# Kernel tuning notes

Measured on AMD Instinct MI355X. Metric: run time of the kernel, lower is better.

Reference implementation:

```python
import jax, jax.numpy as jnp
import numpy as np

NS, NW, E, DIN, OUT, H = 100_000, 400_000, 500_000, 64, 64, 4


def setup_inputs() -> dict:
    key = jax.random.key(0)
    ks = jax.random.split(key, 26)
    s = 1.0 / np.sqrt(DIN)
    sg = 1.0 / np.sqrt(OUT)
    inp = {
        "x_sites": jax.random.normal(ks[0], (NS, DIN), jnp.float32),
        "x_wells": jax.random.normal(ks[1], (NW, DIN), jnp.float32),
        "edge_sw_src": jax.random.randint(ks[2], (E,), 0, NS, jnp.int32),
        "edge_sw_dst": jax.random.randint(ks[3], (E,), 0, NW, jnp.int32),
        "edge_ws_src": jax.random.randint(ks[4], (E,), 0, NW, jnp.int32),
        "edge_ws_dst": jax.random.randint(ks[5], (E,), 0, NS, jnp.int32),
        # GAT ('pfas_sites','distance','gw_wells'), heads=4, concat=False
        "W_sw": jax.random.normal(ks[6], (DIN, H * OUT), jnp.float32) * s,
        "att_src_sw": jax.random.normal(ks[7], (H, OUT), jnp.float32) * sg,
        "att_dst_sw": jax.random.normal(ks[8], (H, OUT), jnp.float32) * sg,
        "b_sw": jnp.zeros((OUT,), jnp.float32),
        # SAGE ('gw_wells','distance','pfas_sites')
        "Wl_ws": jax.random.normal(ks[9], (DIN, OUT), jnp.float32) * s,
        "bl_ws": jnp.zeros((OUT,), jnp.float32),
        "Wr_ws": jax.random.normal(ks[10], (DIN, OUT), jnp.float32) * s,
        # GAT ('pfas_sites','self_loop','pfas_sites'), add_self_loops=True -> identity edges
        "W_ss": jax.random.normal(ks[11], (DIN, H * OUT), jnp.float32) * s,
        "att_src_ss": jax.random.normal(ks[12], (H, OUT), jnp.float32) * sg,
        "att_dst_ss": jax.random.normal(ks[13], (H, OUT), jnp.float32) * sg,
        "b_ss": jnp.zeros((OUT,), jnp.float32),
        # SAGE ('gw_wells','self_loop','gw_wells') with identity edges
        "Wl_ww": jax.random.normal(ks[14], (DIN, OUT), jnp.float32) * s,
        "bl_ww": jnp.zeros((OUT,), jnp.float32),
        "Wr_ww": jax.random.normal(ks[15], (DIN, OUT), jnp.float32) * s,
        # output heads
        "Wg": jax.random.normal(ks[16], (OUT, 1), jnp.float32) * sg,
        "bg": jnp.zeros((1,), jnp.float32),
        "Wsit": jax.random.normal(ks[17], (OUT, 1), jnp.float32) * sg,
        "bsit": jnp.zeros((1,), jnp.float32),
    }
    return inp


def _gat(x_src, x_dst, src, dst, W, a_src, a_dst, b, n_dst):
    """PyG GATConv, concat=False (mean over heads), negative_slope=0.2."""
    h, c = a_src.shape
    xs = (x_src @ W).reshape(-1, h, c)  # [Ns,H,C]
    xd = (x_dst @ W).reshape(-1, h, c)  # [Nd,H,C]
    al_s = jnp.einsum("nhc,hc->nh", xs, a_src)
    al_d = jnp.einsum("nhc,hc->nh", xd, a_dst)
    e = jax.nn.leaky_relu(al_s[src] + al_d[dst], 0.2)  # [E,H]
    m = jax.ops.segment_max(e, dst, num_segments=n_dst)
    ex = jnp.exp(e - m[dst])
    denom = jax.ops.segment_sum(ex, dst, num_segments=n_dst)
    alpha = ex / denom[dst]  # edge-softmax per dst node
    msg = xs[src] * alpha[:, :, None]  # [E,H,C] dominant intermediate
    out = jax.ops.segment_sum(msg, dst, num_segments=n_dst)
    return out.mean(axis=1) + b


def _sage(x_src, x_dst, src, dst, Wl, bl, Wr, n_dst):
    """PyG SAGEConv, mean aggregation, root_weight=True."""
    ssum = jax.ops.segment_sum(x_src[src], dst, num_segments=n_dst)
    cnt = jax.ops.segment_sum(jnp.ones((src.shape[0],), x_src.dtype), dst, num_segments=n_dst)
    mean = ssum / jnp.maximum(cnt, 1.0)[:, None]  # empty neighborhood -> 0 (PyG mean scatter)
    return mean @ Wl + bl + x_dst @ Wr


def reference(x_sites, x_wells, edge_sw_src, edge_sw_dst, edge_ws_src, edge_ws_dst,
              W_sw, att_src_sw, att_dst_sw, b_sw, Wl_ws, bl_ws, Wr_ws,
              W_ss, att_src_ss, att_dst_ss, b_ss, Wl_ww, bl_ww, Wr_ww,
              Wg, bg, Wsit, bsit):
    # relation 1: GAT sites -> wells
    gw = _gat(x_sites, x_wells, edge_sw_src, edge_sw_dst, W_sw, att_src_sw, att_dst_sw, b_sw, NW)
    # relation 4: SAGE self-loop on wells; identity edges -> mean == x itself
    gw = gw + (x_wells @ Wl_ww + bl_ww + x_wells @ Wr_ww)  # HeteroConv aggr='sum'
    # relation 2: SAGE wells -> sites
    si = _sage(x_wells, x_sites, edge_ws_src, edge_ws_dst, Wl_ws, bl_ws, Wr_ws, NS)
    # relation 3: GAT self-loop on sites (add_self_loops=True -> identity edge set);
    # softmax over a single self edge is 1, so output = mean over heads of lin(x) + bias
    si = si + (x_sites @ W_ss).reshape(NS, H, OUT).mean(axis=1) + b_ss
    # post: relu -> dropout (eval mode: identity) -> linear -> leaky_relu(0.01)
    gw = jax.nn.relu(gw)
    si = jax.nn.relu(si)
    o_gw = jax.nn.leaky_relu(gw @ Wg + bg, 0.01)   # [NW, 1]
    o_si = jax.nn.leaky_relu(si @ Wsit + bsit, 0.01)  # [NS, 1]
    return o_gw, o_si
```

## Files before the change

kernel.cpp:

```cpp
#include <hip/hip_runtime.h>

#define NS_ 100000
#define NW_ 400000
#define NE_ 500000
#define EPB 2048

typedef float f32x4_t __attribute__((ext_vector_type(4)));
typedef unsigned u32x4_t __attribute__((ext_vector_type(4)));

__device__ __forceinline__ float lrelu02(float x) { return x > 0.f ? x : 0.2f * x; }
__device__ __forceinline__ float bf2f(unsigned short u) {
    return __uint_as_float(((unsigned)u) << 16);
}
__device__ __forceinline__ unsigned short f2bf(float f) {
    unsigned u = __float_as_uint(f);
    u += 0x7FFFu + ((u >> 16) & 1u);
    return (unsigned short)(u >> 16);
}
__device__ __forceinline__ unsigned pk(float lo, float hi) {
    return (unsigned)f2bf(lo) | ((unsigned)f2bf(hi) << 16);
}
__device__ __forceinline__ void mfma_bf16(f32x4_t& acc, u32x4_t a, u32x4_t b) {
    asm volatile("v_mfma_f32_16x16x32_bf16 %0, %1, %2, %0" : "+v"(acc) : "v"(a), "v"(b));
}

__global__ void __launch_bounds__(256)
k_prep(const float* __restrict__ W_sw, const float* __restrict__ att_src,
       const float* __restrict__ att_dst,
       const float* __restrict__ Wl_ww, const float* __restrict__ Wr_ww,
       const float* __restrict__ Wl_ws, const float* __restrict__ Wr_ws,
       const float* __restrict__ W_ss,
       float* __restrict__ vd, float* __restrict__ vs,
       u32x4_t* __restrict__ fw, u32x4_t* __restrict__ fs,
       u32x4_t* __restrict__ fsp)
{
    const int tid = threadIdx.x;
    {
        int d = tid >> 2, h = tid & 3;
        const float4* wp = (const float4*)(W_sw + d * 256 + h * 64);
        const float4* ad = (const float4*)(att_dst + h * 64);
        const float4* as = (const float4*)(att_src + h * 64);
        float accd = 0.f, accs = 0.f;
#pragma unroll
        for (int c = 0; c < 16; ++c) {
            float4 wv = wp[c]; float4 dv = ad[c]; float4 sv = as[c];
            accd += wv.x * dv.x + wv.y * dv.y + wv.z * dv.z + wv.w * dv.w;
            accs += wv.x * sv.x + wv.y * sv.y + wv.z * sv.z + wv.w * sv.w;
        }
        vd[d * 4 + h] = accd;
        vs[d * 4 + h] = accs;
    }
    for (int idx = tid; idx < 512; idx += 256) {
        int f = idx >> 6, lane = idx & 63;
        int kc = f >> 2, ct = f & 3, q = lane >> 4, n = lane & 15;
        int c = ct * 16 + n;
        u32x4_t d;
#pragma unroll
        for (int i = 0; i < 4; ++i) {
            int k = kc * 32 + q * 8 + 2 * i;
            d[i] = pk(Wl_ww[k * 64 + c] + Wr_ww[k * 64 + c],
                      Wl_ww[(k + 1) * 64 + c] + Wr_ww[(k + 1) * 64 + c]);
        }
        fw[idx] = d;
    }
    for (int idx = tid; idx < 1024; idx += 256) {
        int f = idx >> 6, lane = idx & 63;
        int kc = f >> 2, ct = f & 3, q = lane >> 4, n = lane & 15;
        int c = ct * 16 + n;
        u32x4_t d;
#pragma unroll
        for (int i = 0; i < 4; ++i) {
            int k = kc * 32 + q * 8 + 2 * i;
            float lo, hi;
            if (k < 64) {
                lo = Wl_ws[k * 64 + c];
                hi = Wl_ws[(k + 1) * 64 + c];
            } else {
                int kk = k - 64;
                lo = Wr_ws[kk * 64 + c] + 0.25f * (W_ss[kk * 256 + c] + W_ss[kk * 256 + 64 + c] +
                                                   W_ss[kk * 256 + 128 + c] + W_ss[kk * 256 + 192 + c]);
                hi = Wr_ws[(kk + 1) * 64 + c] + 0.25f * (W_ss[(kk + 1) * 256 + c] + W_ss[(kk + 1) * 256 + 64 + c] +
                                                         W_ss[(kk + 1) * 256 + 128 + c] + W_ss[(kk + 1) * 256 + 192 + c]);
            }
            d[i] = pk(lo, hi);
        }
        fs[idx] = d;
    }
    for (int idx = tid; idx < 2048; idx += 256) {
        int f = idx >> 6, lane = idx & 63;
        int kc = f >> 4, ct = f & 15, q = lane >> 4, n = lane & 15;
        int c = ct * 16 + n;
        u32x4_t d;
#pragma unroll
        for (int i = 0; i < 4; ++i) {
            int k = kc * 32 + q * 8 + 2 * i;
            d[i] = pk(W_sw[k * 256 + c], W_sw[(k + 1) * 256 + c]);
        }
        fsp[idx] = d;
    }
}

#define SP_PAD 264
__global__ void __launch_bounds__(256)
k_sites_pre(const float* __restrict__ x_sites, const u32x4_t* __restrict__ fsp,
            const float* __restrict__ vs, unsigned short* __restrict__ xs,
            float* __restrict__ al_s)
{
    __shared__ unsigned short stg[4][16 * SP_PAD];
    __shared__ float vsl[256];
    const int tid = threadIdx.x;
    vsl[tid] = vs[tid];
    __syncthreads();
    const int wave = __builtin_amdgcn_readfirstlane(tid >> 6);
    const int lane = tid & 63, q = lane >> 4, n = lane & 15;
    const int sbase = blockIdx.x * 64 + wave * 16;
    const int srow = min(sbase + n, NS_ - 1);
    const float* xr = x_sites + (size_t)srow * 64 + q * 8;
    float4 x0 = *(const float4*)(xr);
    float4 x1 = *(const float4*)(xr + 4);
    float4 x2 = *(const float4*)(xr + 32);
    float4 x3 = *(const float4*)(xr + 36);
    u32x4_t am0 = { pk(x0.x, x0.y), pk(x0.z, x0.w), pk(x1.x, x1.y), pk(x1.z, x1.w) };
    u32x4_t am1 = { pk(x2.x, x2.y), pk(x2.z, x2.w), pk(x3.x, x3.y), pk(x3.z, x3.w) };
    float pa[4];
#pragma unroll
    for (int h = 0; h < 4; ++h) {
        const float* v0 = &vsl[(q * 8) * 4 + h];
        const float* v1 = &vsl[(32 + q * 8) * 4 + h];
        pa[h] = x0.x * v0[0]  + x0.y * v0[4]  + x0.z * v0[8]  + x0.w * v0[12]
              + x1.x * v0[16] + x1.y * v0[20] + x1.z * v0[24] + x1.w * v0[28]
              + x2.x * v1[0]  + x2.y * v1[4]  + x2.z * v1[8]  + x2.w * v1[12]
              + x3.x * v1[16] + x3.y * v1[20] + x3.z * v1[24] + x3.w * v1[28];
    }
#pragma unroll
    for (int h = 0; h < 4; ++h) {
        pa[h] += __shfl_xor(pa[h], 16, 64);
        pa[h] += __shfl_xor(pa[h], 32, 64);
    }
    if (q == 0 && sbase + n < NS_)
        *(float4*)(al_s + (size_t)(sbase + n) * 4) = make_float4(pa[0], pa[1], pa[2], pa[3]);

    f32x4_t acc[16];
#pragma unroll
    for (int ct = 0; ct < 16; ++ct) acc[ct] = (f32x4_t){0, 0, 0, 0};
    asm volatile("s_nop 3" : "+v"(am0), "+v"(am1));
#pragma unroll
    for (int ct = 0; ct < 16; ++ct) mfma_bf16(acc[ct], am0, fsp[ct * 64 + lane]);
#pragma unroll
    for (int ct = 0; ct < 16; ++ct) mfma_bf16(acc[ct], am1, fsp[(16 + ct) * 64 + lane]);
    asm volatile("s_nop 7\n\ts_nop 7" ::: "memory");
    unsigned short* ss = &stg[wave][0];
#pragma unroll
    for (int ct = 0; ct < 16; ++ct)
#pragma unroll
        for (int reg = 0; reg < 4; ++reg)
            ss[(q * 4 + reg) * SP_PAD + ct * 16 + n] = f2bf(acc[ct][reg]);
    __builtin_amdgcn_s_waitcnt(0);
#pragma unroll
    for (int i = 0; i < 8; ++i) {
        int g = i * 64 + lane;
        int r = g >> 5, c = g & 31;
        if (sbase + r < NS_) {
            u32x4_t v = *(const u32x4_t*)(ss + r * SP_PAD + c * 8);
            *(u32x4_t*)(xs + (size_t)(sbase + r) * 256 + c * 8) = v;
        }
    }
}

__global__ void __launch_bounds__(256)
k_hist2(const int* __restrict__ d1, int* __restrict__ h1,
        const int* __restrict__ d2, int* __restrict__ h2)
{
    int e = blockIdx.x * 256 + threadIdx.x;
    if (e >= NE_) return;
    if (blockIdx.y == 0) atomicAdd(&h1[d1[e]], 1);
    else                 atomicAdd(&h2[d2[e]], 1);
}

__global__ void __launch_bounds__(256)
k_scan1_2(const int* __restrict__ h1, int n1, int* __restrict__ b1, int nb1,
          const int* __restrict__ h2, int n2, int* __restrict__ b2)
{
    __shared__ int red[256];
    const int tid = threadIdx.x;
    const int bx = blockIdx.x;
    const int* hist; int n; int* bsum; int blk;
    if (bx < nb1) { hist = h1; n = n1; bsum = b1; blk = bx; }
    else          { hist = h2; n = n2; bsum = b2; blk = bx - nb1; }
    int base = blk * EPB + tid * 8;
    int s = 0;
#pragma unroll
    for (int i = 0; i < 8; ++i) { int idx = base + i; if (idx < n) s += hist[idx]; }
    red[tid] = s;
    __syncthreads();
    for (int off = 128; off > 0; off >>= 1) {
        if (tid < off) red[tid] += red[tid + off];
        __syncthreads();
    }
    if (tid == 0) bsum[blk] = red[0];
}

__global__ void __launch_bounds__(256)
k_scan2_2(int* __restrict__ b1, int nb1, int* __restrict__ b2, int nb2)
{
    __shared__ int sh[256];
    const int tid = threadIdx.x;
    int* bsum = blockIdx.x == 0 ? b1 : b2;
    int nb = blockIdx.x == 0 ? nb1 : nb2;
    sh[tid] = (tid < nb) ? bsum[tid] : 0;
    __syncthreads();
    for (int off = 1; off < 256; off <<= 1) {
        int u = (tid >= off) ? sh[tid - off] : 0;
        __syncthreads();
        sh[tid] += u;
        __syncthreads();
    }
    if (tid < nb) bsum[tid] = (tid == 0) ? 0 : sh[tid - 1];
}

__global__ void __launch_bounds__(256)
k_scan3_2(const int* __restrict__ h1, int n1, const int* __restrict__ b1,
          int* __restrict__ rp1, int* __restrict__ cu1, int nb1,
          const int* __restrict__ h2, int n2, const int* __restrict__ b2,
          int* __restrict__ rp2, int* __restrict__ cu2)
{
    __shared__ int tsum[256];
    const int tid = threadIdx.x;
    const int bx = blockIdx.x;
    const int* hist; int n; const int* bsum; int* rowptr; int* cursor; int blk;
    if (bx < nb1) { hist = h1; n = n1; bsum = b1; rowptr = rp1; cursor = cu1; blk = bx; }
    else          { hist = h2; n = n2; bsum = b2; rowptr = rp2; cursor = cu2; blk = bx - nb1; }
    int base = blk * EPB + tid * 8;
    int v[8]; int s = 0;
#pragma unroll
    for (int i = 0; i < 8; ++i) {
        int idx = base + i;
        v[i] = (idx < n) ? hist[idx] : 0;
        s += v[i];
    }
    tsum[tid] = s;
    __syncthreads();
    for (int off = 1; off < 256; off <<= 1) {
        int u = (tid >= off) ? tsum[tid - off] : 0;
        __syncthreads();
        tsum[tid] += u;
        __syncthreads();
    }
    int texcl = tsum[tid] - s;
    int run = bsum[blk] + texcl;
#pragma unroll
    for (int i = 0; i < 8; ++i) {
        int idx = base + i;
        if (idx < n) { rowptr[idx] = run; cursor[idx] = run; run += v[i]; }
    }
    if (blk == 0 && tid == 0) rowptr[n] = NE_;
}

__global__ void __launch_bounds__(256)
k_scatter2(const int* __restrict__ s1, const int* __restrict__ d1,
           int* __restrict__ c1, int* __restrict__ o1,
           const int* __restrict__ s2, const int* __restrict__ d2,
           int* __restrict__ c2, int* __restrict__ o2)
{
    int e = blockIdx.x * 256 + threadIdx.x;
    if (e >= NE_) return;
    if (blockIdx.y == 0) { int p = atomicAdd(&c1[d1[e]], 1); o1[p] = s1[e]; }
    else                 { int p = atomicAdd(&c2[d2[e]], 1); o2[p] = s2[e]; }
}

__global__ void __launch_bounds__(256)
k_gat_wells(const float* __restrict__ x_wells, const float* __restrict__ vd,
            const int* __restrict__ rowptr, const int* __restrict__ csr_src,
            const float* __restrict__ al_s, const unsigned short* __restrict__ xs,
            const float* __restrict__ b_sw, const float* __restrict__ bl_ww,
            const u32x4_t* __restrict__ fw, const float* __restrict__ Wg,
            const float* __restrict__ bg, float* __restrict__ out)
{
    __shared__ float vdl[16][17];
    __shared__ float xw[16][68];
    __shared__ float dl[16][68];
    __shared__ float biasl[64];
    __shared__ float wgl[64];
    __shared__ float res[16];
    const int tid = threadIdx.x;
    vdl[tid >> 4][tid & 15] = vd[tid];
    if (tid < 64) { biasl[tid] = b_sw[tid] + bl_ww[tid]; wgl[tid] = Wg[tid]; }
    __syncthreads();
    const int wl = tid >> 4, p = tid & 15;
    const int w = blockIdx.x * 16 + wl;
    float h0, h1, h2, h3;
    {
        float4 xv = *(const float4*)(x_wells + (size_t)w * 64 + 4 * p);
        *(float4*)&xw[wl][4 * p] = xv;
        const float* vp = vdl[p];
        h0 = xv.x * vp[0] + xv.y * vp[4] + xv.z * vp[8]  + xv.w * vp[12];
        h1 = xv.x * vp[1] + xv.y * vp[5] + xv.z * vp[9]  + xv.w * vp[13];
        h2 = xv.x * vp[2] + xv.y * vp[6] + xv.z * vp[10] + xv.w * vp[14];
        h3 = xv.x * vp[3] + xv.y * vp[7] + xv.z * vp[11] + xv.w * vp[15];
    }
#pragma unroll
    for (int off = 1; off < 16; off <<= 1) {
        h0 += __shfl_xor(h0, off, 64);
        h1 += __shfl_xor(h1, off, 64);
        h2 += __shfl_xor(h2, off, 64);
        h3 += __shfl_xor(h3, off, 64);
    }
    const int r0 = rowptr[w], r1 = rowptr[w + 1];
    float den0 = 0, den1 = 0, den2 = 0, den3 = 0;
    float n0[4] = {0, 0, 0, 0}, n1[4] = {0, 0, 0, 0};
    float n2[4] = {0, 0, 0, 0}, n3[4] = {0, 0, 0, 0};
    for (int j = r0; j < r1; ++j) {
        int s = csr_src[j];
        float4 as = ((const float4*)al_s)[s];
        float e0 = __expf(lrelu02(as.x + h0));
        float e1 = __expf(lrelu02(as.y + h1));
        float e2 = __expf(lrelu02(as.z + h2));
        float e3 = __expf(lrelu02(as.w + h3));
        den0 += e0; den1 += e1; den2 += e2; den3 += e3;
        const unsigned short* xr = xs + (size_t)s * 256 + 4 * p;
        ushort4 u0 = *(const ushort4*)(xr);
        ushort4 u1 = *(const ushort4*)(xr + 64);
        ushort4 u2 = *(const ushort4*)(xr + 128);
        ushort4 u3 = *(const ushort4*)(xr + 192);
        n0[0] += e0 * bf2f(u0.x); n0[1] += e0 * bf2f(u0.y); n0[2] += e0 * bf2f(u0.z); n0[3] += e0 * bf2f(u0.w);
        n1[0] += e1 * bf2f(u1.x); n1[1] += e1 * bf2f(u1.y); n1[2] += e1 * bf2f(u1.z); n1[3] += e1 * bf2f(u1.w);
        n2[0] += e2 * bf2f(u2.x); n2[1] += e2 * bf2f(u2.y); n2[2] += e2 * bf2f(u2.z); n2[3] += e2 * bf2f(u2.w);
        n3[0] += e3 * bf2f(u3.x); n3[1] += e3 * bf2f(u3.y); n3[2] += e3 * bf2f(u3.z); n3[3] += e3 * bf2f(u3.w);
    }
    const int c0 = 4 * p;
    float tmsg[4];
    if (r1 > r0) {
        float i0 = 0.25f / den0, i1 = 0.25f / den1, i2 = 0.25f / den2, i3 = 0.25f / den3;
#pragma unroll
        for (int i = 0; i < 4; ++i)
            tmsg[i] = n0[i] * i0 + n1[i] * i1 + n2[i] * i2 + n3[i] * i3 + biasl[c0 + i];
    } else {
#pragma unroll
        for (int i = 0; i < 4; ++i) tmsg[i] = biasl[c0 + i];
    }
    __syncthreads();
    const int wave = __builtin_amdgcn_readfirstlane(tid >> 6);
    const int lane = tid & 63, q = lane >> 4, n = lane & 15;
    u32x4_t a0, a1;
#pragma unroll
    for (int i = 0; i < 4; ++i) {
        a0[i] = pk(xw[n][q * 8 + 2 * i],      xw[n][q * 8 + 2 * i + 1]);
        a1[i] = pk(xw[n][32 + q * 8 + 2 * i], xw[n][32 + q * 8 + 2 * i + 1]);
    }
    f32x4_t acc = {0, 0, 0, 0};
    asm volatile("s_nop 3" : "+v"(a0), "+v"(a1), "+v"(acc));
    mfma_bf16(acc, a0, fw[wave * 64 + lane]);
    mfma_bf16(acc, a1, fw[(4 + wave) * 64 + lane]);
    asm volatile("s_nop 7\n\ts_nop 7" : "+v"(acc));
#pragma unroll
    for (int reg = 0; reg < 4; ++reg)
        dl[q * 4 + reg][wave * 16 + n] = acc[reg];
    __syncthreads();
    float4 dv = *(const float4*)&dl[wl][c0];
    float t0 = tmsg[0] + dv.x;
    float t1 = tmsg[1] + dv.y;
    float t2 = tmsg[2] + dv.z;
    float t3 = tmsg[3] + dv.w;
    float pr = fmaxf(t0, 0.f) * wgl[c0] + fmaxf(t1, 0.f) * wgl[c0 + 1] +
               fmaxf(t2, 0.f) * wgl[c0 + 2] + fmaxf(t3, 0.f) * wgl[c0 + 3];
    pr += __shfl_xor(pr, 1, 64);
    pr += __shfl_xor(pr, 2, 64);
    pr += __shfl_xor(pr, 4, 64);
    pr += __shfl_xor(pr, 8, 64);
    if (p == 0) res[wl] = pr + bg[0];
    __syncthreads();
    if (tid < 16) {
        float v = res[tid];
        out[blockIdx.x * 16 + tid] = v > 0.f ? v : 0.01f * v;
    }
}

__global__ void __launch_bounds__(256)
k_sage_sites(const float* __restrict__ x_sites, const float* __restrict__ x_wells,
             const int* __restrict__ rowptr, const int* __restrict__ csr_src,
             const u32x4_t* __restrict__ fs, const float* __restrict__ bl_ws,
             const float* __restrict__ b_ss, const float* __restrict__ Wsit,
             const float* __restrict__ bsit, float* __restrict__ out)
{
    __shared__ float mnL[16][68];
    __shared__ float xL[16][68];
    __shared__ float dl[16][68];
    __shared__ float biasl[64];
    __shared__ float wsl[64];
    __shared__ float res[16];
    const int tid = threadIdx.x;
    if (tid < 64) { biasl[tid] = bl_ws[tid] + b_ss[tid]; wsl[tid] = Wsit[tid]; }
    const int sl = tid >> 4, p = tid & 15;
    const int s = blockIdx.x * 16 + sl;
    const int r0 = rowptr[s], r1 = rowptr[s + 1];
    float4 m4 = {0.f, 0.f, 0.f, 0.f};
    for (int j = r0; j < r1; ++j) {
        int wsrc = csr_src[j];
        float4 xv = ((const float4*)(x_wells + (size_t)wsrc * 64))[p];
        m4.x += xv.x; m4.y += xv.y; m4.z += xv.z; m4.w += xv.w;
    }
    if (r1 > r0) {
        float rc = 1.f / (float)(r1 - r0);
        m4.x *= rc; m4.y *= rc; m4.z *= rc; m4.w *= rc;
    }
    *(float4*)&mnL[sl][4 * p] = m4;
    {
        float4 xv = *(const float4*)(x_sites + (size_t)s * 64 + 4 * p);
        *(float4*)&xL[sl][4 * p] = xv;
    }
    __syncthreads();
    const int wave = __builtin_amdgcn_readfirstlane(tid >> 6);
    const int lane = tid & 63, q = lane >> 4, n = lane & 15;
    u32x4_t am0, am1, ax0, ax1;
#pragma unroll
    for (int i = 0; i < 4; ++i) {
        am0[i] = pk(mnL[n][q * 8 + 2 * i],      mnL[n][q * 8 + 2 * i + 1]);
        am1[i] = pk(mnL[n][32 + q * 8 + 2 * i], mnL[n][32 + q * 8 + 2 * i + 1]);
        ax0[i] = pk(xL[n][q * 8 + 2 * i],       xL[n][q * 8 + 2 * i + 1]);
        ax1[i] = pk(xL[n][32 + q * 8 + 2 * i],  xL[n][32 + q * 8 + 2 * i + 1]);
    }
    f32x4_t acc = {0, 0, 0, 0};
    asm volatile("s_nop 3" : "+v"(am0), "+v"(am1), "+v"(ax0), "+v"(ax1), "+v"(acc));
    mfma_bf16(acc, am0, fs[wave * 64 + lane]);
    mfma_bf16(acc, am1, fs[(4 + wave) * 64 + lane]);
    mfma_bf16(acc, ax0, fs[(8 + wave) * 64 + lane]);
    mfma_bf16(acc, ax1, fs[(12 + wave) * 64 + lane]);
    asm volatile("s_nop 7\n\ts_nop 7" : "+v"(acc));
#pragma unroll
    for (int reg = 0; reg < 4; ++reg)
        dl[q * 4 + reg][wave * 16 + n] = acc[reg];
    __syncthreads();
    const int c0 = 4 * p;
    float4 dv = *(const float4*)&dl[sl][c0];
    float t0 = dv.x + biasl[c0];
    float t1 = dv.y + biasl[c0 + 1];
    float t2 = dv.z + biasl[c0 + 2];
    float t3 = dv.w + biasl[c0 + 3];
    float pr = fmaxf(t0, 0.f) * wsl[c0] + fmaxf(t1, 0.f) * wsl[c0 + 1] +
               fmaxf(t2, 0.f) * wsl[c0 + 2] + fmaxf(t3, 0.f) * wsl[c0 + 3];
    pr += __shfl_xor(pr, 1, 64);
    pr += __shfl_xor(pr, 2, 64);
    pr += __shfl_xor(pr, 4, 64);
    pr += __shfl_xor(pr, 8, 64);
    if (p == 0) res[sl] = pr + bsit[0];
    __syncthreads();
    if (tid < 16) {
        float v = res[tid];
        out[(size_t)NW_ + blockIdx.x * 16 + tid] = v > 0.f ? v : 0.01f * v;
    }
}

extern "C" void kernel_launch(void* const* d_in, const int* in_sizes, int n_in,
                              void* d_out, int out_size, void* d_ws, size_t ws_size,
                              hipStream_t stream)
{
    const float* x_sites    = (const float*)d_in[0];
    const float* x_wells    = (const float*)d_in[1];
    const int*   e_sw_src   = (const int*)d_in[2];
    const int*   e_sw_dst   = (const int*)d_in[3];
    const int*   e_ws_src   = (const int*)d_in[4];
    const int*   e_ws_dst   = (const int*)d_in[5];
    const float* W_sw       = (const float*)d_in[6];
    const float* att_src_sw = (const float*)d_in[7];
    const float* att_dst_sw = (const float*)d_in[8];
    const float* b_sw       = (const float*)d_in[9];
    const float* Wl_ws      = (const float*)d_in[10];
    const float* bl_ws      = (const float*)d_in[11];
    const float* Wr_ws      = (const float*)d_in[12];
    const float* W_ss       = (const float*)d_in[13];
    const float* b_ss       = (const float*)d_in[16];
    const float* Wl_ww      = (const float*)d_in[17];
    const float* bl_ww      = (const float*)d_in[18];
    const float* Wr_ww      = (const float*)d_in[19];
    const float* Wg         = (const float*)d_in[20];
    const float* bg         = (const float*)d_in[21];
    const float* Wsit       = (const float*)d_in[22];
    const float* bsit       = (const float*)d_in[23];
    float* out = (float*)d_out;

    unsigned short* xs = (unsigned short*)d_ws;
    float* al_s = (float*)(xs + (size_t)NS_ * 256);
    float* vd   = al_s + (size_t)NS_ * 4;
    float* vs   = vd + 256;
    u32x4_t* fw = (u32x4_t*)(vs + 256);
    u32x4_t* fs = fw + 512;
    u32x4_t* fsp= fs + 1024;
    int* ip     = (int*)(fsp + 2048);
    int* h_sw   = ip;
    int* h_ws   = h_sw + NW_;
    int* rp_sw  = h_ws + NS_;
    int* cur_sw = rp_sw + NW_ + 4;
    int* csr_sw = cur_sw + NW_;
    int* bs_sw  = csr_sw + NE_;
    int* rp_ws  = bs_sw + 256;
    int* cur_ws = rp_ws + NS_ + 4;
    int* csr_ws = cur_ws + NS_;
    int* bs_ws  = csr_ws + NE_;

    hipMemsetAsync(h_sw, 0, (size_t)(NW_ + NS_) * sizeof(int), stream);

    const int egrid = (NE_ + 255) / 256;
    const int nb_sw = (NW_ + EPB - 1) / EPB;
    const int nb_ws = (NS_ + EPB - 1) / EPB;

    hipLaunchKernelGGL(k_hist2, dim3(egrid, 2), dim3(256), 0, stream,
                       e_sw_dst, h_sw, e_ws_dst, h_ws);
    hipLaunchKernelGGL(k_scan1_2, dim3(nb_sw + nb_ws), dim3(256), 0, stream,
                       h_sw, NW_, bs_sw, nb_sw, h_ws, NS_, bs_ws);
    hipLaunchKernelGGL(k_scan2_2, dim3(2), dim3(256), 0, stream,
                       bs_sw, nb_sw, bs_ws, nb_ws);
    hipLaunchKernelGGL(k_scan3_2, dim3(nb_sw + nb_ws), dim3(256), 0, stream,
                       h_sw, NW_, bs_sw, rp_sw, cur_sw, nb_sw,
                       h_ws, NS_, bs_ws, rp_ws, cur_ws);
    hipLaunchKernelGGL(k_scatter2, dim3(egrid, 2), dim3(256), 0, stream,
                       e_sw_src, e_sw_dst, cur_sw, csr_sw,
                       e_ws_src, e_ws_dst, cur_ws, csr_ws);

    hipLaunchKernelGGL(k_prep, dim3(1), dim3(256), 0, stream,
                       W_sw, att_src_sw, att_dst_sw, Wl_ww, Wr_ww, Wl_ws, Wr_ws, W_ss,
                       vd, vs, fw, fs, fsp);
    hipLaunchKernelGGL(k_sites_pre, dim3((NS_ + 63) / 64), dim3(256), 0, stream,
                       x_sites, fsp, vs, xs, al_s);

    hipLaunchKernelGGL(k_gat_wells, dim3(NW_ / 16), dim3(256), 0, stream,
                       x_wells, vd, rp_sw, csr_sw, al_s, xs, b_sw, bl_ww,
                       fw, Wg, bg, out);
    hipLaunchKernelGGL(k_sage_sites, dim3(NS_ / 16), dim3(256), 0, stream,
                       x_sites, x_wells, rp_ws, csr_ws, fs, bl_ws, b_ss,
                       Wsit, bsit, out);
}
```

Baseline: 468.5 us.

## Aggregate raw site features per head, apply GAT projection after aggregation

Sites are no longer projected to a 256-wide bf16 per-head buffer up front. Only a 64-wide bf16 copy of x_sites plus the attention logits is written. The wells kernel aggregates attention-weighted raw features per head into a 256-wide LDS tile, then projects it with eight extra MFMAs against a head-stacked W_sw fragment. This cuts the per-edge gather from four 8-byte reads to one and shrinks the intermediate buffer fourfold, in exchange for more MFMA work and LDS per wells block. The SAGE kernel also packs its bf16 operands into LDS directly instead of repacking from float tiles.

```diff
diff --git a/kernel.cpp b/kernel.cpp
--- a/kernel.cpp
+++ b/kernel.cpp
@@ -32,7 +32,7 @@
        const float* __restrict__ W_ss,
        float* __restrict__ vd, float* __restrict__ vs,
        u32x4_t* __restrict__ fw, u32x4_t* __restrict__ fs,
-       u32x4_t* __restrict__ fsp)
+       u32x4_t* __restrict__ fgw)
 {
     const int tid = threadIdx.x;
     {
@@ -88,83 +88,56 @@
     }
     for (int idx = tid; idx < 2048; idx += 256) {
         int f = idx >> 6, lane = idx & 63;
-        int kc = f >> 4, ct = f & 15, q = lane >> 4, n = lane & 15;
+        int kc = f >> 2, ct = f & 3, q = lane >> 4, n = lane & 15;
         int c = ct * 16 + n;
         u32x4_t d;
 #pragma unroll
         for (int i = 0; i < 4; ++i) {
-            int k = kc * 32 + q * 8 + 2 * i;
-            d[i] = pk(W_sw[k * 256 + c], W_sw[(k + 1) * 256 + c]);
+            int kk = kc * 32 + q * 8 + 2 * i;
+            int h = kk >> 6, k0 = kk & 63;
+            d[i] = pk(W_sw[k0 * 256 + h * 64 + c], W_sw[(k0 + 1) * 256 + h * 64 + c]);
         }
-        fsp[idx] = d;
-    }
-}
-
-#define SP_PAD 264
-__global__ void __launch_bounds__(256)
-k_sites_pre(const float* __restrict__ x_sites, const u32x4_t* __restrict__ fsp,
-            const float* __restrict__ vs, unsigned short* __restrict__ xs,
-            float* __restrict__ al_s)
-{
-    __shared__ unsigned short stg[4][16 * SP_PAD];
+        fgw[idx] = d;
+    }
+}
+
+__global__ void __launch_bounds__(256)
+k_sites_al(const float* __restrict__ x_sites, const float* __restrict__ vs,
+           unsigned short* __restrict__ xbf, float* __restrict__ al_s)
+{
     __shared__ float vsl[256];
     const int tid = threadIdx.x;
     vsl[tid] = vs[tid];
     __syncthreads();
-    const int wave = __builtin_amdgcn_readfirstlane(tid >> 6);
-    const int lane = tid & 63, q = lane >> 4, n = lane & 15;
-    const int sbase = blockIdx.x * 64 + wave * 16;
-    const int srow = min(sbase + n, NS_ - 1);
-    const float* xr = x_sites + (size_t)srow * 64 + q * 8;
-    float4 x0 = *(const float4*)(xr);
-    float4 x1 = *(const float4*)(xr + 4);
-    float4 x2 = *(const float4*)(xr + 32);
-    float4 x3 = *(const float4*)(xr + 36);
-    u32x4_t am0 = { pk(x0.x, x0.y), pk(x0.z, x0.w), pk(x1.x, x1.y), pk(x1.z, x1.w) };
-    u32x4_t am1 = { pk(x2.x, x2.y), pk(x2.z, x2.w), pk(x3.x, x3.y), pk(x3.z, x3.w) };
+    const int s = blockIdx.x * 64 + (tid >> 2);
+    const int qq = tid & 3;
+    if (s >= NS_) return;
+    const float* xr = x_sites + (size_t)s * 64 + qq * 16;
+    float4 a = *(const float4*)(xr);
+    float4 b = *(const float4*)(xr + 4);
+    float4 c = *(const float4*)(xr + 8);
+    float4 d = *(const float4*)(xr + 12);
     float pa[4];
 #pragma unroll
     for (int h = 0; h < 4; ++h) {
-        const float* v0 = &vsl[(q * 8) * 4 + h];
-        const float* v1 = &vsl[(32 + q * 8) * 4 + h];
-        pa[h] = x0.x * v0[0]  + x0.y * v0[4]  + x0.z * v0[8]  + x0.w * v0[12]
-              + x1.x * v0[16] + x1.y * v0[20] + x1.z * v0[24] + x1.w * v0[28]
-              + x2.x * v1[0]  + x2.y * v1[4]  + x2.z * v1[8]  + x2.w * v1[12]
-              + x3.x * v1[16] + x3.y * v1[20] + x3.z * v1[24] + x3.w * v1[28];
+        const float* v = &vsl[(qq * 16) * 4 + h];
+        pa[h] = a.x * v[0]  + a.y * v[4]  + a.z * v[8]  + a.w * v[12]
+              + b.x * v[16] + b.y * v[20] + b.z * v[24] + b.w * v[28]
+              + c.x * v[32] + c.y * v[36] + c.z * v[40] + c.w * v[44]
+              + d.x * v[48] + d.y * v[52] + d.z * v[56] + d.w * v[60];
     }
 #pragma unroll
     for (int h = 0; h < 4; ++h) {
-        pa[h] += __shfl_xor(pa[h], 16, 64);
-        pa[h] += __shfl_xor(pa[h], 32, 64);
-    }
-    if (q == 0 && sbase + n < NS_)
-        *(float4*)(al_s + (size_t)(sbase + n) * 4) = make_float4(pa[0], pa[1], pa[2], pa[3]);
-
-    f32x4_t acc[16];
-#pragma unroll
-    for (int ct = 0; ct < 16; ++ct) acc[ct] = (f32x4_t){0, 0, 0, 0};
-    asm volatile("s_nop 3" : "+v"(am0), "+v"(am1));
-#pragma unroll
-    for (int ct = 0; ct < 16; ++ct) mfma_bf16(acc[ct], am0, fsp[ct * 64 + lane]);
-#pragma unroll
-    for (int ct = 0; ct < 16; ++ct) mfma_bf16(acc[ct], am1, fsp[(16 + ct) * 64 + lane]);
-    asm volatile("s_nop 7\n\ts_nop 7" ::: "memory");
-    unsigned short* ss = &stg[wave][0];
-#pragma unroll
-    for (int ct = 0; ct < 16; ++ct)
-#pragma unroll
-        for (int reg = 0; reg < 4; ++reg)
-            ss[(q * 4 + reg) * SP_PAD + ct * 16 + n] = f2bf(acc[ct][reg]);
-    __builtin_amdgcn_s_waitcnt(0);
-#pragma unroll
-    for (int i = 0; i < 8; ++i) {
-        int g = i * 64 + lane;
-        int r = g >> 5, c = g & 31;
-        if (sbase + r < NS_) {
-            u32x4_t v = *(const u32x4_t*)(ss + r * SP_PAD + c * 8);
-            *(u32x4_t*)(xs + (size_t)(sbase + r) * 256 + c * 8) = v;
-        }
-    }
+        pa[h] += __shfl_xor(pa[h], 1, 64);
+        pa[h] += __shfl_xor(pa[h], 2, 64);
+    }
+    if (qq == 0)
+        *(float4*)(al_s + (size_t)s * 4) = make_float4(pa[0], pa[1], pa[2], pa[3]);
+    u32x4_t lo = { pk(a.x, a.y), pk(a.z, a.w), pk(b.x, b.y), pk(b.z, b.w) };
+    u32x4_t hi = { pk(c.x, c.y), pk(c.z, c.w), pk(d.x, d.y), pk(d.z, d.w) };
+    unsigned short* xo = xbf + (size_t)s * 64 + qq * 16;
+    *(u32x4_t*)(xo) = lo;
+    *(u32x4_t*)(xo + 8) = hi;
 }
 
 __global__ void __launch_bounds__(256)
@@ -271,13 +244,15 @@
 __global__ void __launch_bounds__(256)
 k_gat_wells(const float* __restrict__ x_wells, const float* __restrict__ vd,
             const int* __restrict__ rowptr, const int* __restrict__ csr_src,
-            const float* __restrict__ al_s, const unsigned short* __restrict__ xs,
+            const float* __restrict__ al_s, const unsigned short* __restrict__ xbf,
             const float* __restrict__ b_sw, const float* __restrict__ bl_ww,
-            const u32x4_t* __restrict__ fw, const float* __restrict__ Wg,
-            const float* __restrict__ bg, float* __restrict__ out)
+            const u32x4_t* __restrict__ fw, const u32x4_t* __restrict__ fgw,
+            const float* __restrict__ Wg, const float* __restrict__ bg,
+            float* __restrict__ out)
 {
     __shared__ float vdl[16][17];
-    __shared__ float xw[16][68];
+    __shared__ unsigned xwB[16][36];
+    __shared__ unsigned agB[16][132];
     __shared__ float dl[16][68];
     __shared__ float biasl[64];
     __shared__ float wgl[64];
@@ -291,7 +266,7 @@
     float h0, h1, h2, h3;
     {
         float4 xv = *(const float4*)(x_wells + (size_t)w * 64 + 4 * p);
-        *(float4*)&xw[wl][4 * p] = xv;
+        *(uint2*)&xwB[wl][2 * p] = make_uint2(pk(xv.x, xv.y), pk(xv.z, xv.w));
         const float* vp = vdl[p];
         h0 = xv.x * vp[0] + xv.y * vp[4] + xv.z * vp[8]  + xv.w * vp[12];
         h1 = xv.x * vp[1] + xv.y * vp[5] + xv.z * vp[9]  + xv.w * vp[13];
@@ -307,60 +282,59 @@
     }
     const int r0 = rowptr[w], r1 = rowptr[w + 1];
     float den0 = 0, den1 = 0, den2 = 0, den3 = 0;
-    float n0[4] = {0, 0, 0, 0}, n1[4] = {0, 0, 0, 0};
-    float n2[4] = {0, 0, 0, 0}, n3[4] = {0, 0, 0, 0};
+    float a00=0,a01=0,a02=0,a03=0, a10=0,a11=0,a12=0,a13=0;
+    float a20=0,a21=0,a22=0,a23=0, a30=0,a31=0,a32=0,a33=0;
     for (int j = r0; j < r1; ++j) {
         int s = csr_src[j];
         float4 as = ((const float4*)al_s)[s];
+        ushort4 u = *(const ushort4*)(xbf + (size_t)s * 64 + 4 * p);
         float e0 = __expf(lrelu02(as.x + h0));
         float e1 = __expf(lrelu02(as.y + h1));
         float e2 = __expf(lrelu02(as.z + h2));
         float e3 = __expf(lrelu02(as.w + h3));
         den0 += e0; den1 += e1; den2 += e2; den3 += e3;
-        const unsigned short* xr = xs + (size_t)s * 256 + 4 * p;
-        ushort4 u0 = *(const ushort4*)(xr);
-        ushort4 u1 = *(const ushort4*)(xr + 64);
-        ushort4 u2 = *(const ushort4*)(xr + 128);
-        ushort4 u3 = *(const ushort4*)(xr + 192);
-        n0[0] += e0 * bf2f(u0.x); n0[1] += e0 * bf2f(u0.y); n0[2] += e0 * bf2f(u0.z); n0[3] += e0 * bf2f(u0.w);
-        n1[0] += e1 * bf2f(u1.x); n1[1] += e1 * bf2f(u1.y); n1[2] += e1 * bf2f(u1.z); n1[3] += e1 * bf2f(u1.w);
-        n2[0] += e2 * bf2f(u2.x); n2[1] += e2 * bf2f(u2.y); n2[2] += e2 * bf2f(u2.z); n2[3] += e2 * bf2f(u2.w);
-        n3[0] += e3 * bf2f(u3.x); n3[1] += e3 * bf2f(u3.y); n3[2] += e3 * bf2f(u3.z); n3[3] += e3 * bf2f(u3.w);
-    }
-    const int c0 = 4 * p;
-    float tmsg[4];
+        float x0 = bf2f(u.x), x1 = bf2f(u.y), x2 = bf2f(u.z), x3 = bf2f(u.w);
+        a00 += e0 * x0; a01 += e0 * x1; a02 += e0 * x2; a03 += e0 * x3;
+        a10 += e1 * x0; a11 += e1 * x1; a12 += e1 * x2; a13 += e1 * x3;
+        a20 += e2 * x0; a21 += e2 * x1; a22 += e2 * x2; a23 += e2 * x3;
+        a30 += e3 * x0; a31 += e3 * x1; a32 += e3 * x2; a33 += e3 * x3;
+    }
     if (r1 > r0) {
         float i0 = 0.25f / den0, i1 = 0.25f / den1, i2 = 0.25f / den2, i3 = 0.25f / den3;
-#pragma unroll
-        for (int i = 0; i < 4; ++i)
-            tmsg[i] = n0[i] * i0 + n1[i] * i1 + n2[i] * i2 + n3[i] * i3 + biasl[c0 + i];
-    } else {
-#pragma unroll
-        for (int i = 0; i < 4; ++i) tmsg[i] = biasl[c0 + i];
-    }
+        a00 *= i0; a01 *= i0; a02 *= i0; a03 *= i0;
+        a10 *= i1; a11 *= i1; a12 *= i1; a13 *= i1;
+        a20 *= i2; a21 *= i2; a22 *= i2; a23 *= i2;
+        a30 *= i3; a31 *= i3; a32 *= i3; a33 *= i3;
+    }
+    *(uint2*)&agB[wl][0 * 32 + 2 * p] = make_uint2(pk(a00, a01), pk(a02, a03));
+    *(uint2*)&agB[wl][1 * 32 + 2 * p] = make_uint2(pk(a10, a11), pk(a12, a13));
+    *(uint2*)&agB[wl][2 * 32 + 2 * p] = make_uint2(pk(a20, a21), pk(a22, a23));
+    *(uint2*)&agB[wl][3 * 32 + 2 * p] = make_uint2(pk(a30, a31), pk(a32, a33));
     __syncthreads();
     const int wave = __builtin_amdgcn_readfirstlane(tid >> 6);
     const int lane = tid & 63, q = lane >> 4, n = lane & 15;
-    u32x4_t a0, a1;
-#pragma unroll
-    for (int i = 0; i < 4; ++i) {
-        a0[i] = pk(xw[n][q * 8 + 2 * i],      xw[n][q * 8 + 2 * i + 1]);
-        a1[i] = pk(xw[n][32 + q * 8 + 2 * i], xw[n][32 + q * 8 + 2 * i + 1]);
-    }
+    u32x4_t ax0 = *(const u32x4_t*)&xwB[n][q * 4];
+    u32x4_t ax1 = *(const u32x4_t*)&xwB[n][16 + q * 4];
     f32x4_t acc = {0, 0, 0, 0};
-    asm volatile("s_nop 3" : "+v"(a0), "+v"(a1), "+v"(acc));
-    mfma_bf16(acc, a0, fw[wave * 64 + lane]);
-    mfma_bf16(acc, a1, fw[(4 + wave) * 64 + lane]);
+    asm volatile("s_nop 3" : "+v"(ax0), "+v"(ax1), "+v"(acc));
+    mfma_bf16(acc, ax0, fw[wave * 64 + lane]);
+    mfma_bf16(acc, ax1, fw[(4 + wave) * 64 + lane]);
+#pragma unroll
+    for (int kc = 0; kc < 8; ++kc) {
+        u32x4_t a = *(const u32x4_t*)&agB[n][kc * 16 + q * 4];
+        mfma_bf16(acc, a, fgw[(kc * 4 + wave) * 64 + lane]);
+    }
     asm volatile("s_nop 7\n\ts_nop 7" : "+v"(acc));
 #pragma unroll
     for (int reg = 0; reg < 4; ++reg)
         dl[q * 4 + reg][wave * 16 + n] = acc[reg];
     __syncthreads();
+    const int c0 = 4 * p;
     float4 dv = *(const float4*)&dl[wl][c0];
-    float t0 = tmsg[0] + dv.x;
-    float t1 = tmsg[1] + dv.y;
-    float t2 = tmsg[2] + dv.z;
-    float t3 = tmsg[3] + dv.w;
+    float t0 = dv.x + biasl[c0];
+    float t1 = dv.y + biasl[c0 + 1];
+    float t2 = dv.z + biasl[c0 + 2];
+    float t3 = dv.w + biasl[c0 + 3];
     float pr = fmaxf(t0, 0.f) * wgl[c0] + fmaxf(t1, 0.f) * wgl[c0 + 1] +
                fmaxf(t2, 0.f) * wgl[c0 + 2] + fmaxf(t3, 0.f) * wgl[c0 + 3];
     pr += __shfl_xor(pr, 1, 64);
@@ -382,8 +356,8 @@
              const float* __restrict__ b_ss, const float* __restrict__ Wsit,
              const float* __restrict__ bsit, float* __restrict__ out)
 {
-    __shared__ float mnL[16][68];
-    __shared__ float xL[16][68];
+    __shared__ unsigned mnB[16][36];
+    __shared__ unsigned xB[16][36];
     __shared__ float dl[16][68];
     __shared__ float biasl[64];
     __shared__ float wsl[64];
@@ -403,22 +377,18 @@
         float rc = 1.f / (float)(r1 - r0);
         m4.x *= rc; m4.y *= rc; m4.z *= rc; m4.w *= rc;
     }
-    *(float4*)&mnL[sl][4 * p] = m4;
+    *(uint2*)&mnB[sl][2 * p] = make_uint2(pk(m4.x, m4.y), pk(m4.z, m4.w));
     {
         float4 xv = *(const float4*)(x_sites + (size_t)s * 64 + 4 * p);
-        *(float4*)&xL[sl][4 * p] = xv;
+        *(uint2*)&xB[sl][2 * p] = make_uint2(pk(xv.x, xv.y), pk(xv.z, xv.w));
     }
     __syncthreads();
     const int wave = __builtin_amdgcn_readfirstlane(tid >> 6);
     const int lane = tid & 63, q = lane >> 4, n = lane & 15;
-    u32x4_t am0, am1, ax0, ax1;
-#pragma unroll
-    for (int i = 0; i < 4; ++i) {
-        am0[i] = pk(mnL[n][q * 8 + 2 * i],      mnL[n][q * 8 + 2 * i + 1]);
-        am1[i] = pk(mnL[n][32 + q * 8 + 2 * i], mnL[n][32 + q * 8 + 2 * i + 1]);
-        ax0[i] = pk(xL[n][q * 8 + 2 * i],       xL[n][q * 8 + 2 * i + 1]);
-        ax1[i] = pk(xL[n][32 + q * 8 + 2 * i],  xL[n][32 + q * 8 + 2 * i + 1]);
-    }
+    u32x4_t am0 = *(const u32x4_t*)&mnB[n][q * 4];
+    u32x4_t am1 = *(const u32x4_t*)&mnB[n][16 + q * 4];
+    u32x4_t ax0 = *(const u32x4_t*)&xB[n][q * 4];
+    u32x4_t ax1 = *(const u32x4_t*)&xB[n][16 + q * 4];
     f32x4_t acc = {0, 0, 0, 0};
     asm volatile("s_nop 3" : "+v"(am0), "+v"(am1), "+v"(ax0), "+v"(ax1), "+v"(acc));
     mfma_bf16(acc, am0, fs[wave * 64 + lane]);
@@ -478,14 +448,14 @@
     const float* bsit       = (const float*)d_in[23];
     float* out = (float*)d_out;
 
-    unsigned short* xs = (unsigned short*)d_ws;
-    float* al_s = (float*)(xs + (size_t)NS_ * 256);
+    unsigned short* xbf = (unsigned short*)d_ws;
+    float* al_s = (float*)(xbf + (size_t)NS_ * 64);
     float* vd   = al_s + (size_t)NS_ * 4;
     float* vs   = vd + 256;
     u32x4_t* fw = (u32x4_t*)(vs + 256);
     u32x4_t* fs = fw + 512;
-    u32x4_t* fsp= fs + 1024;
-    int* ip     = (int*)(fsp + 2048);
+    u32x4_t* fgw= fs + 1024;
+    int* ip     = (int*)(fgw + 2048);
     int* h_sw   = ip;
     int* h_ws   = h_sw + NW_;
     int* rp_sw  = h_ws + NS_;
@@ -518,13 +488,13 @@
 
     hipLaunchKernelGGL(k_prep, dim3(1), dim3(256), 0, stream,
                        W_sw, att_src_sw, att_dst_sw, Wl_ww, Wr_ww, Wl_ws, Wr_ws, W_ss,
-                       vd, vs, fw, fs, fsp);
-    hipLaunchKernelGGL(k_sites_pre, dim3((NS_ + 63) / 64), dim3(256), 0, stream,
-                       x_sites, fsp, vs, xs, al_s);
+                       vd, vs, fw, fs, fgw);
+    hipLaunchKernelGGL(k_sites_al, dim3((NS_ + 63) / 64), dim3(256), 0, stream,
+                       x_sites, vs, xbf, al_s);
 
     hipLaunchKernelGGL(k_gat_wells, dim3(NW_ / 16), dim3(256), 0, stream,
-                       x_wells, vd, rp_sw, csr_sw, al_s, xs, b_sw, bl_ww,
-                       fw, Wg, bg, out);
+                       x_wells, vd, rp_sw, csr_sw, al_s, xbf, b_sw, bl_ww,
+                       fw, fgw, Wg, bg, out);
     hipLaunchKernelGGL(k_sage_sites, dim3(NS_ / 16), dim3(256), 0, stream,
                        x_sites, x_wells, rp_ws, csr_ws, fs, bl_ws, b_ss,
                        Wsit, bsit, out);
```

Measured after the change: 464.7 us. About the same (-0.8%).
